# Performance work log

Hardware: AMD Instinct MI355X
Metric: run time of the kernel (lower is better)

Reference implementation:

```python
import jax, jax.numpy as jnp
import numpy as np

N_EMBD = 1024
N_HEAD = 16
HEAD_DIM = N_EMBD // N_HEAD  # 64
N_CTX = 2048
ROPE_THETA = 10000.0


def _rope_cache(L, dim, base):
    inv_freq = 1.0 / (base ** (np.arange(0, dim, 2, dtype=np.float32) / dim))
    t = np.arange(L, dtype=np.float32)
    freqs = np.einsum('i,j->ij', t, inv_freq)  # (L, dim/2)
    return jnp.asarray(np.cos(freqs)), jnp.asarray(np.sin(freqs))


def _apply_rotary(x, cos, sin):
    # x: (B, H, L, D), cos/sin: (L, D/2) -> broadcast (1,1,L,D/2)
    x1 = x[..., ::2]
    x2 = x[..., 1::2]
    c = cos[None, None, :, :]
    s = sin[None, None, :, :]
    y1 = x1 * c - x2 * s
    y2 = x1 * s + x2 * c
    # interleave back: stack on last dim then flatten
    return jnp.stack((y1, y2), axis=-1).reshape(x.shape)


def setup_inputs() -> dict:
    key = jax.random.key(0)
    k1, k2, k3, k4, k5 = jax.random.split(key, 5)
    B, L, D = 4, 2048, N_EMBD
    scale = 0.02
    x = jax.random.normal(k1, (B, L, D), dtype=jnp.float32)
    W_qkv = jax.random.normal(k2, (D, 3 * D), dtype=jnp.float32) * scale
    b_qkv = jnp.zeros((3 * D,), dtype=jnp.float32)
    W_proj = jax.random.normal(k3, (D, D), dtype=jnp.float32) * scale
    b_proj = jnp.zeros((D,), dtype=jnp.float32)
    attention_mask = jnp.ones((B, L), dtype=jnp.int32)
    return {"x": x, "W_qkv": W_qkv, "b_qkv": b_qkv, "W_proj": W_proj,
            "b_proj": b_proj, "attention_mask": attention_mask}


def reference(x, W_qkv, b_qkv, W_proj, b_proj, attention_mask):
    B, L, D = x.shape
    H, Dh = N_HEAD, HEAD_DIM
    qkv = x @ W_qkv + b_qkv  # (B, L, 3D)
    q, k, v = jnp.split(qkv, 3, axis=2)
    # (B, L, H, Dh) -> (B, H, L, Dh)
    q = q.reshape(B, L, H, Dh).transpose(0, 2, 1, 3)
    k = k.reshape(B, L, H, Dh).transpose(0, 2, 1, 3)
    v = v.reshape(B, L, H, Dh).transpose(0, 2, 1, 3)
    cos, sin = _rope_cache(L, Dh, ROPE_THETA)
    q = _apply_rotary(q, cos, sin)
    k = _apply_rotary(k, cos, sin)
    # mask: causal & key padding keep
    causal = jnp.tril(jnp.ones((L, L), dtype=bool))[None, None]        # (1,1,L,L)
    key_keep = attention_mask.astype(bool)[:, None, None, :]          # (B,1,1,L)
    keep = causal & key_keep                                          # (B,1,L,L)
    scores = jnp.einsum('bhqd,bhkd->bhqk', q, k) / jnp.sqrt(jnp.float32(Dh))
    scores = jnp.where(keep, scores, jnp.finfo(scores.dtype).min)
    attn = jax.nn.softmax(scores, axis=-1)
    out = jnp.einsum('bhqk,bhkd->bhqd', attn, v)  # (B,H,L,Dh)
    out = out.transpose(0, 2, 1, 3).reshape(B, L, D)
    return out @ W_proj + b_proj
```

## Files before the change

kernel.cpp:

```cpp
#include <hip/hip_runtime.h>
#include <math.h>

typedef __bf16 bf16x8 __attribute__((ext_vector_type(8)));
typedef float f32x4 __attribute__((ext_vector_type(4)));
typedef float f32x16 __attribute__((ext_vector_type(16)));
typedef unsigned short u16;
typedef unsigned short u16x8 __attribute__((ext_vector_type(8)));
typedef unsigned short u16x4 __attribute__((ext_vector_type(4)));
typedef unsigned u32x2v __attribute__((ext_vector_type(2)));

#define BATCH 4
#define SEQ   2048
#define EMBD  1024
#define NHEAD 16
#define HDIM  64
#define MROWS 8192
#define QKVN  3072

__device__ __forceinline__ u16 f2bf(float f) {
    union { float f; unsigned u; } cv; cv.f = f;
    unsigned u = cv.u;
    return (u16)((u + 0x7FFFu + ((u >> 16) & 1u)) >> 16);
}

__device__ __forceinline__ unsigned cvtpk_bf16(float lo, float hi) {
    unsigned r;
    asm("v_cvt_pk_bf16_f32 %0, %1, %2" : "=v"(r) : "v"(lo), "v"(hi));
    return r;
}

__device__ __forceinline__ void glds16(const void* g, void* l) {
    __builtin_amdgcn_global_load_lds(
        (const __attribute__((address_space(1))) unsigned int*)(g),
        (__attribute__((address_space(3))) unsigned int*)(l), 16, 0, 0);
}

__device__ __forceinline__ void transpose_body(const float* __restrict__ W,
                                               u16* __restrict__ Wt, int K, int N,
                                               int n0, int k0, u16 (*T)[68]) {
    const int tx = threadIdx.x & 15, ty = threadIdx.x >> 4;
#pragma unroll
    for (int r = 0; r < 4; r++) {
        int k = k0 + ty + r * 16;
        float4 w = *(const float4*)&W[(size_t)k * N + n0 + tx * 4];
        T[tx * 4 + 0][ty + r * 16] = f2bf(w.x);
        T[tx * 4 + 1][ty + r * 16] = f2bf(w.y);
        T[tx * 4 + 2][ty + r * 16] = f2bf(w.z);
        T[tx * 4 + 3][ty + r * 16] = f2bf(w.w);
    }
    __syncthreads();
#pragma unroll
    for (int r = 0; r < 4; r++) {
        int nl = ty + r * 16;
        u16x4 v = { T[nl][tx * 4 + 0], T[nl][tx * 4 + 1],
                    T[nl][tx * 4 + 2], T[nl][tx * 4 + 3] };
        *(u16x4*)&Wt[(size_t)(n0 + nl) * K + k0 + tx * 4] = v;
    }
}

__global__ __launch_bounds__(256)
void prep_kernel(const float* __restrict__ x, const float* __restrict__ Wqkv,
                 const float* __restrict__ Wproj, const int* __restrict__ amask,
                 u16* __restrict__ Xb, u16* __restrict__ Wqkvt, u16* __restrict__ Wprojt,
                 float* __restrict__ ropeC, float* __restrict__ ropeS,
                 float* __restrict__ mbias, int* __restrict__ flags) {
    __shared__ union { u16 T[64][68]; int ok[4]; } sm;
    const int bx = blockIdx.x, tid = threadIdx.x;
    if (bx < 8192) {
        int i = bx * 256 + tid;
        float4 v = ((const float4*)x)[i];
        u16x4 o = { f2bf(v.x), f2bf(v.y), f2bf(v.z), f2bf(v.w) };
        ((u16x4*)Xb)[i] = o;
    } else if (bx < 8960) {
        int bxx = bx - 8192;
        transpose_body(Wqkv, Wqkvt, EMBD, QKVN, (bxx % 48) * 64, (bxx / 48) * 64, sm.T);
    } else if (bx < 9216) {
        int bxx = bx - 8960;
        transpose_body(Wproj, Wprojt, EMBD, EMBD, (bxx & 15) * 64, (bxx >> 4) * 64, sm.T);
    } else if (bx < 9472) {
        int i = (bx - 9216) * 256 + tid;
        int l = i >> 5, p = i & 31;
        float invf = powf(10000.0f, -(float)(2 * p) * (1.0f / 64.0f));
        float sv, cv;
        sincosf((float)l * invf, &sv, &cv);
        ropeC[i] = cv; ropeS[i] = sv;
    } else {
        int idx = (bx - 9472) * 256 + tid;
        int mv = amask[idx];
        mbias[idx] = mv ? 0.0f : -1e30f;
        unsigned long long bal = __ballot(mv != 0);
        int wv = tid >> 6;
        if ((tid & 63) == 0) sm.ok[wv] = (bal == 0xFFFFFFFFFFFFFFFFull);
        __syncthreads();
        if (tid == 0)   flags[idx >> 7] = sm.ok[0] & sm.ok[1];
        if (tid == 128) flags[idx >> 7] = sm.ok[2] & sm.ok[3];
    }
}

__global__ __launch_bounds__(256)
void qkv_gemm(const u16* __restrict__ A, const u16* __restrict__ Bt,
              const float* __restrict__ bias,
              const float* __restrict__ Ct, const float* __restrict__ St,
              u16* __restrict__ Qo, u16* __restrict__ Ko, u16* __restrict__ Vo) {
    __shared__ u16 As[128 * 32];
    __shared__ u16 Bs[128 * 32];
    const int tid = threadIdx.x;
    const int wv = tid >> 6, ln = tid & 63;
    const int quad = ln >> 4, l16 = ln & 15;
    const int m0 = blockIdx.y * 128, n0 = blockIdx.x * 128;
    const int wm = wv >> 1, wn = wv & 1;

    f32x4 acc[4][4] = {};
    for (int k0 = 0; k0 < EMBD; k0 += 32) {
#pragma unroll
        for (int p = 0; p < 2; p++) {
            int slot = p * 256 + tid;
            int row = slot >> 2, ch = slot & 3;
            glds16(A  + (size_t)(m0 + row) * EMBD + k0 + ch * 8, As + (p * 256 + wv * 64) * 8);
            glds16(Bt + (size_t)(n0 + row) * EMBD + k0 + ch * 8, Bs + (p * 256 + wv * 64) * 8);
        }
        __syncthreads();
        bf16x8 af[4], bfr[4];
#pragma unroll
        for (int i = 0; i < 4; i++) af[i]  = *(const bf16x8*)&As[(wm * 64 + i * 16 + l16) * 32 + quad * 8];
#pragma unroll
        for (int j = 0; j < 4; j++) bfr[j] = *(const bf16x8*)&Bs[(wn * 64 + j * 16 + l16) * 32 + quad * 8];
#pragma unroll
        for (int i = 0; i < 4; i++)
#pragma unroll
            for (int j = 0; j < 4; j++)
                acc[i][j] = __builtin_amdgcn_mfma_f32_16x16x32_bf16(af[i], bfr[j], acc[i][j], 0, 0, 0);
        __syncthreads();
    }

    const int sec = n0 >> 10;
    if (sec == 2) {
#pragma unroll
        for (int i = 0; i < 4; i++)
#pragma unroll
            for (int r = 0; r < 4; r++) {
                int m = m0 + wm * 64 + i * 16 + quad * 4 + r;
                int b = m >> 11, l = m & 2047;
#pragma unroll
                for (int j = 0; j < 4; j++) {
                    int n = n0 + wn * 64 + j * 16 + l16;
                    int dcol = n & 1023;
                    int h = dcol >> 6, dh = dcol & 63;
                    float v = acc[i][j][r] + bias[n];
                    Vo[(((size_t)b * NHEAD + h) * SEQ + l) * HDIM + dh] = f2bf(v);
                }
            }
    } else {
        u16* O = (sec == 0) ? Qo : Ko;
        const float qs = (sec == 0) ? 0.125f * 1.44269504f : 1.0f;
#pragma unroll
        for (int i = 0; i < 4; i++)
#pragma unroll
            for (int r = 0; r < 4; r++) {
                int m = m0 + wm * 64 + i * 16 + quad * 4 + r;
                int b = m >> 11, l = m & 2047;
#pragma unroll
                for (int j = 0; j < 4; j++) {
                    int n = n0 + wn * 64 + j * 16 + l16;
                    int h = (n & 1023) >> 6, dh = n & 63;
                    int p = (n & 63) >> 1;
                    float v = acc[i][j][r] + bias[n];
                    float pv = __shfl_xor(v, 1, 64);
                    float cv = Ct[l * 32 + p], sv = St[l * 32 + p];
                    float o = (l16 & 1) ? (pv * sv + v * cv) : (v * cv - pv * sv);
                    O[(((size_t)b * NHEAD + h) * SEQ + l) * HDIM + dh] = f2bf(o * qs);
                }
            }
    }
}

__global__ __launch_bounds__(256)
void transpose_v(const u16* __restrict__ Vo, u16* __restrict__ Vt) {
    __shared__ u16 T[64][72];
    const int bh = blockIdx.y;
    const int l0 = blockIdx.x * 64;
    const int tx = threadIdx.x & 15, ty = threadIdx.x >> 4;
#pragma unroll
    for (int rr = 0; rr < 4; rr++) {
        int l = ty + rr * 16;
        u16x4 v = *(const u16x4*)&Vo[((size_t)bh * SEQ + l0 + l) * HDIM + tx * 4];
        T[l][tx * 4 + 0] = v.x; T[l][tx * 4 + 1] = v.y;
        T[l][tx * 4 + 2] = v.z; T[l][tx * 4 + 3] = v.w;
    }
    __syncthreads();
#pragma unroll
    for (int rr = 0; rr < 4; rr++) {
        int dh = ty + rr * 16;
        u16x4 w = { T[tx * 4 + 0][dh], T[tx * 4 + 1][dh],
                    T[tx * 4 + 2][dh], T[tx * 4 + 3][dh] };
        *(u16x4*)&Vt[((size_t)bh * HDIM + dh) * SEQ + l0 + tx * 4] = w;
    }
}

__global__ __launch_bounds__(256)
void attn_mfma3(const u16* __restrict__ Qb, const u16* __restrict__ Kb,
                const u16* __restrict__ Vt, const float* __restrict__ mb,
                const int* __restrict__ flags, u16* __restrict__ Ot) {
    __shared__ u16 SM[32768];
    const int tid = threadIdx.x;
    const int wv = tid >> 6, ln = tid & 63;
    const int l32 = ln & 31, hi = ln >> 5;
    const int bh = blockIdx.x & 63;
    const int pr = blockIdx.x >> 6;
    const int b = bh >> 4;
    const u16* Qg = Qb + (size_t)bh * SEQ * HDIM;
    const u16* Kg = Kb + (size_t)bh * SEQ * HDIM;
    const u16* Vg = Vt + (size_t)bh * HDIM * SEQ;

    const int kRow = ln >> 3;
    const size_t kLane = (size_t)(wv * 32 + kRow) * 64 + ((ln & 7) ^ kRow) * 8;
    const int vRow = ln >> 4, sc0 = (ln & 15) ^ vRow;
    const size_t vLaneE = (size_t)(wv * 16 + vRow) * SEQ + sc0 * 8;
    const size_t vLaneO = (size_t)(wv * 16 + vRow) * SEQ + (sc0 ^ 4) * 8;

    for (int pass = 0; pass < 2; pass++) {
        const int qt = pass ? pr : 15 - pr;
        const int q0w = qt * 128 + wv * 32;

        bf16x8 Qf[4];
#pragma unroll
        for (int kd = 0; kd < 4; kd++)
            Qf[kd] = *(const bf16x8*)&Qg[(size_t)(q0w + l32) * HDIM + kd * 16 + hi * 8];

        f32x16 o[2] = {};
        float mrun = -1e30f, lrun = 0.f;

        {
            u16* KsD = SM + wv * 2048;
            u16* VsD = SM + 8192 + wv * 2048;
#pragma unroll
            for (int p = 0; p < 4; p++) {
                glds16(Kg + kLane + p * 512, KsD + p * 512);
                glds16(Vg + ((p & 1) ? vLaneO : vLaneE) + (size_t)p * 4 * SEQ, VsD + p * 512);
            }
        }
        __syncthreads();

        int buf = 0;
        for (int kt = 0; kt <= qt; kt++) {
            const int kbase = kt * 128;
            if (kt < qt) {
                const size_t nb = (size_t)(kbase + 128);
                u16* KsD = SM + (buf ^ 1) * 16384 + wv * 2048;
                u16* VsD = SM + (buf ^ 1) * 16384 + 8192 + wv * 2048;
#pragma unroll
                for (int p = 0; p < 4; p++) {
                    glds16(Kg + nb * 64 + kLane + p * 512, KsD + p * 512);
                    glds16(Vg + nb + ((p & 1) ? vLaneO : vLaneE) + (size_t)p * 4 * SEQ, VsD + p * 512);
                }
            }
            const u16* Ks = SM + buf * 16384;
            const u16* Vs = SM + buf * 16384 + 8192;

            f32x16 s[4];
            __builtin_amdgcn_s_setprio(1);
#pragma unroll
            for (int mi = 0; mi < 4; mi++) {
                const int key = mi * 32 + l32;
                f32x16 z = {};
#pragma unroll
                for (int kd = 0; kd < 4; kd++) {
                    int ch = kd * 2 + hi;
                    bf16x8 kf = *(const bf16x8*)&Ks[key * 64 + ((ch ^ (key & 7)) * 8)];
                    z = __builtin_amdgcn_mfma_f32_32x32x16_bf16(kf, Qf[kd], z, 0, 0, 0);
                }
                s[mi] = z;
            }
            __builtin_amdgcn_s_setprio(0);

            if (kt == qt) {
                const int qloc = wv * 32 + l32;
#pragma unroll
                for (int mi = 0; mi < 4; mi++)
#pragma unroll
                    for (int r = 0; r < 16; r++) {
                        int row = mi * 32 + (r & 3) + 8 * (r >> 2) + 4 * hi;
                        if (row > qloc) s[mi][r] = -1e30f;
                    }
            }
            if (!flags[b * 16 + kt]) {
#pragma unroll
                for (int mi = 0; mi < 4; mi++)
#pragma unroll
                    for (int r = 0; r < 16; r++) {
                        int row = mi * 32 + (r & 3) + 8 * (r >> 2) + 4 * hi;
                        s[mi][r] += mb[b * SEQ + kbase + row];
                    }
            }

            float rm = -1e30f;
#pragma unroll
            for (int mi = 0; mi < 4; mi++) {
                float a0 = fmaxf(fmaxf(s[mi][0],  s[mi][1]),  fmaxf(s[mi][2],  s[mi][3]));
                float a1 = fmaxf(fmaxf(s[mi][4],  s[mi][5]),  fmaxf(s[mi][6],  s[mi][7]));
                float a2 = fmaxf(fmaxf(s[mi][8],  s[mi][9]),  fmaxf(s[mi][10], s[mi][11]));
                float a3 = fmaxf(fmaxf(s[mi][12], s[mi][13]), fmaxf(s[mi][14], s[mi][15]));
                rm = fmaxf(rm, fmaxf(fmaxf(a0, a1), fmaxf(a2, a3)));
            }
            {
                u32x2v f = __builtin_amdgcn_permlane32_swap(
                    __float_as_uint(rm), __float_as_uint(rm), false, false);
                rm = fmaxf(__uint_as_float(f[0]), __uint_as_float(f[1]));
            }
            if (!__all(rm <= mrun + 8.0f)) {
                float mnew = fmaxf(mrun, rm);
                float al = __builtin_amdgcn_exp2f(mrun - mnew);
                mrun = mnew;
                lrun *= al;
#pragma unroll
                for (int r = 0; r < 16; r++) { o[0][r] *= al; o[1][r] *= al; }
            }
            float rs = 0.f;
#pragma unroll
            for (int mi = 0; mi < 4; mi++) {
                float ps = 0.f;
#pragma unroll
                for (int r = 0; r < 16; r++) {
                    float pe = __builtin_amdgcn_exp2f(s[mi][r] - mrun);
                    s[mi][r] = pe;
                    ps += pe;
                }
                rs += ps;
            }
            {
                u32x2v f = __builtin_amdgcn_permlane32_swap(
                    __float_as_uint(rs), __float_as_uint(rs), false, false);
                rs = __uint_as_float(f[0]) + __uint_as_float(f[1]);
            }
            lrun += rs;

#pragma unroll
            for (int t = 0; t < 4; t++) {
                unsigned A0 = cvtpk_bf16(s[t][0],  s[t][1]);
                unsigned B0 = cvtpk_bf16(s[t][4],  s[t][5]);
                unsigned A1 = cvtpk_bf16(s[t][2],  s[t][3]);
                unsigned B1 = cvtpk_bf16(s[t][6],  s[t][7]);
                u32x2v r0 = __builtin_amdgcn_permlane32_swap(A0, B0, false, false);
                u32x2v r1 = __builtin_amdgcn_permlane32_swap(A1, B1, false, false);
                union { unsigned u[4]; bf16x8 v; } p0;
                p0.u[0] = r0[0]; p0.u[1] = r1[0]; p0.u[2] = r0[1]; p0.u[3] = r1[1];

                unsigned A2 = cvtpk_bf16(s[t][8],  s[t][9]);
                unsigned B2 = cvtpk_bf16(s[t][12], s[t][13]);
                unsigned A3 = cvtpk_bf16(s[t][10], s[t][11]);
                unsigned B3 = cvtpk_bf16(s[t][14], s[t][15]);
                u32x2v r2 = __builtin_amdgcn_permlane32_swap(A2, B2, false, false);
                u32x2v r3 = __builtin_amdgcn_permlane32_swap(A3, B3, false, false);
                union { unsigned u[4]; bf16x8 v; } p1;
                p1.u[0] = r2[0]; p1.u[1] = r3[0]; p1.u[2] = r2[1]; p1.u[3] = r3[1];

                __builtin_amdgcn_s_setprio(1);
#pragma unroll
                for (int md = 0; md < 2; md++) {
                    const int dh = md * 32 + l32;
                    bf16x8 v0 = *(const bf16x8*)&Vs[dh * 128 + (((t * 4 + hi)     ^ (dh & 7)) * 8)];
                    o[md] = __builtin_amdgcn_mfma_f32_32x32x16_bf16(v0, p0.v, o[md], 0, 0, 0);
                    bf16x8 v1 = *(const bf16x8*)&Vs[dh * 128 + (((t * 4 + 2 + hi) ^ (dh & 7)) * 8)];
                    o[md] = __builtin_amdgcn_mfma_f32_32x32x16_bf16(v1, p1.v, o[md], 0, 0, 0);
                }
                __builtin_amdgcn_s_setprio(0);
            }
            __syncthreads();
            buf ^= 1;
        }

        u16* Osh = SM + wv * 2176;
        float inv = 1.0f / lrun;
#pragma unroll
        for (int md = 0; md < 2; md++)
#pragma unroll
            for (int r = 0; r < 16; r++) {
                int dh = md * 32 + (r & 3) + 8 * (r >> 2) + 4 * hi;
                Osh[l32 * 68 + dh] = f2bf(o[md][r] * inv);
            }
        __syncthreads();
        {
            int qrow = ln >> 1, hf = ln & 1;
            size_t gbase = ((size_t)bh * SEQ + qt * 128 + wv * 32 + qrow) * HDIM + hf * 32;
#pragma unroll
            for (int c = 0; c < 4; c++) {
                u16x8 vv = *(const u16x8*)&Osh[qrow * 68 + hf * 32 + c * 8];
                *(u16x8*)&Ot[gbase + c * 8] = vv;
            }
        }
        __syncthreads();
    }
}

__global__ __launch_bounds__(256)
void proj_gemm(const u16* __restrict__ A, const u16* __restrict__ Bt,
               const float* __restrict__ bias, float* __restrict__ out) {
    __shared__ u16 As[128 * 32];
    __shared__ u16 Bs[128 * 32];
    const int tid = threadIdx.x;
    const int wv = tid >> 6, ln = tid & 63;
    const int quad = ln >> 4, l16 = ln & 15;
    const int m0 = blockIdx.y * 128, n0 = blockIdx.x * 128;
    const int wm = wv >> 1, wn = wv & 1;

    f32x4 acc[4][4] = {};
    for (int k0 = 0; k0 < EMBD; k0 += 32) {
#pragma unroll
        for (int p = 0; p < 2; p++) {
            int slot = p * 256 + tid;
            int row = slot >> 2, ch = slot & 3;
            int m = m0 + row;
            int bb = m >> 11, l = m & 2047;
            int hh = k0 >> 6;
            glds16(A + (((size_t)(bb * 16 + hh) * SEQ + l) * HDIM) + (k0 & 63) + ch * 8,
                   As + (p * 256 + wv * 64) * 8);
            glds16(Bt + (size_t)(n0 + row) * EMBD + k0 + ch * 8, Bs + (p * 256 + wv * 64) * 8);
        }
        __syncthreads();
        bf16x8 af[4], bfr[4];
#pragma unroll
        for (int i = 0; i < 4; i++) af[i]  = *(const bf16x8*)&As[(wm * 64 + i * 16 + l16) * 32 + quad * 8];
#pragma unroll
        for (int j = 0; j < 4; j++) bfr[j] = *(const bf16x8*)&Bs[(wn * 64 + j * 16 + l16) * 32 + quad * 8];
#pragma unroll
        for (int i = 0; i < 4; i++)
#pragma unroll
            for (int j = 0; j < 4; j++)
                acc[i][j] = __builtin_amdgcn_mfma_f32_16x16x32_bf16(af[i], bfr[j], acc[i][j], 0, 0, 0);
        __syncthreads();
    }
#pragma unroll
    for (int i = 0; i < 4; i++)
#pragma unroll
        for (int r = 0; r < 4; r++) {
            int m = m0 + wm * 64 + i * 16 + quad * 4 + r;
#pragma unroll
            for (int j = 0; j < 4; j++) {
                int n = n0 + wn * 64 + j * 16 + l16;
                out[(size_t)m * EMBD + n] = acc[i][j][r] + bias[n];
            }
        }
}

extern "C" void kernel_launch(void* const* d_in, const int* in_sizes, int n_in,
                              void* d_out, int out_size, void* d_ws, size_t ws_size,
                              hipStream_t stream)
{
    const float* x     = (const float*)d_in[0];
    const float* Wqkv  = (const float*)d_in[1];
    const float* bqkv  = (const float*)d_in[2];
    const float* Wproj = (const float*)d_in[3];
    const float* bproj = (const float*)d_in[4];
    const int*   amask = (const int*)d_in[5];
    float* out = (float*)d_out;

    char* ws = (char*)d_ws;
    u16*   Xb     = (u16*)(ws);
    u16*   Ot     = (u16*)(ws);
    u16*   Wqkvt  = (u16*)(ws + 16777216);
    u16*   Wprojt = (u16*)(ws + 23068672);
    u16*   Qb     = (u16*)(ws + 25165824);
    u16*   Kb     = (u16*)(ws + 41943040);
    u16*   Vb     = (u16*)(ws + 58720256);
    u16*   Vtp    = (u16*)(ws + 75497472);
    float* ropeC  = (float*)(ws + 92274688);
    float* ropeS  = (float*)(ws + 92536832);
    float* mbias  = (float*)(ws + 92798976);
    int*   flags  = (int*)(ws + 92831744);

    prep_kernel<<<9504, 256, 0, stream>>>(x, Wqkv, Wproj, amask,
                                          Xb, Wqkvt, Wprojt, ropeC, ropeS, mbias, flags);
    qkv_gemm<<<dim3(QKVN / 128, MROWS / 128), 256, 0, stream>>>(
        Xb, Wqkvt, bqkv, ropeC, ropeS, Qb, Kb, Vb);
    transpose_v<<<dim3(32, 64), 256, 0, stream>>>(Vb, Vtp);
    attn_mfma3<<<512, 256, 0, stream>>>(Qb, Kb, Vtp, mbias, flags, Ot);
    proj_gemm<<<dim3(EMBD / 128, MROWS / 128), 256, 0, stream>>>(Ot, Wprojt, bproj, out);
}
```

Measured before the change: 278.9 us.

## Double-buffer GEMM K-tiles with XOR-swizzled LDS and block-index swizzle

```diff
diff --git a/kernel.cpp b/kernel.cpp
--- a/kernel.cpp
+++ b/kernel.cpp
@@ -102,35 +102,61 @@
               const float* __restrict__ bias,
               const float* __restrict__ Ct, const float* __restrict__ St,
               u16* __restrict__ Qo, u16* __restrict__ Ko, u16* __restrict__ Vo) {
-    __shared__ u16 As[128 * 32];
-    __shared__ u16 Bs[128 * 32];
+    __shared__ u16 SM[32768];
     const int tid = threadIdx.x;
     const int wv = tid >> 6, ln = tid & 63;
     const int quad = ln >> 4, l16 = ln & 15;
-    const int m0 = blockIdx.y * 128, n0 = blockIdx.x * 128;
+    const int bid = blockIdx.y * 24 + blockIdx.x;
+    const int swz = (bid & 7) * 192 + (bid >> 3);
+    const int m0 = (swz / 24) * 128, n0 = (swz % 24) * 128;
     const int wm = wv >> 1, wn = wv & 1;
 
+    const int srow = wv * 8 + (ln >> 3);
+    const int xs = (ln & 7) ^ (srow & 7);
+
     f32x4 acc[4][4] = {};
-    for (int k0 = 0; k0 < EMBD; k0 += 32) {
-#pragma unroll
-        for (int p = 0; p < 2; p++) {
-            int slot = p * 256 + tid;
-            int row = slot >> 2, ch = slot & 3;
-            glds16(A  + (size_t)(m0 + row) * EMBD + k0 + ch * 8, As + (p * 256 + wv * 64) * 8);
-            glds16(Bt + (size_t)(n0 + row) * EMBD + k0 + ch * 8, Bs + (p * 256 + wv * 64) * 8);
-        }
+
+    auto stage = [&](int buf, int k0) {
+        u16* As = SM + buf * 16384;
+        u16* Bs = As + 8192;
+#pragma unroll
+        for (int p = 0; p < 4; p++) {
+            int row = p * 32 + srow;
+            glds16(A  + (size_t)(m0 + row) * EMBD + k0 + xs * 8, As + (p * 256 + wv * 64) * 8);
+            glds16(Bt + (size_t)(n0 + row) * EMBD + k0 + xs * 8, Bs + (p * 256 + wv * 64) * 8);
+        }
+    };
+
+    stage(0, 0);
+    __syncthreads();
+    int buf = 0;
+    for (int kt = 0; kt < 16; kt++) {
+        if (kt < 15) stage(buf ^ 1, (kt + 1) * 64);
+        const u16* As = SM + buf * 16384;
+        const u16* Bs = As + 8192;
+        __builtin_amdgcn_s_setprio(1);
+#pragma unroll
+        for (int kk = 0; kk < 2; kk++) {
+            bf16x8 af[4], bfr[4];
+#pragma unroll
+            for (int i = 0; i < 4; i++) {
+                int R = wm * 64 + i * 16 + l16;
+                af[i] = *(const bf16x8*)&As[R * 64 + (((kk * 4 + quad) ^ (R & 7)) * 8)];
+            }
+#pragma unroll
+            for (int j = 0; j < 4; j++) {
+                int R = wn * 64 + j * 16 + l16;
+                bfr[j] = *(const bf16x8*)&Bs[R * 64 + (((kk * 4 + quad) ^ (R & 7)) * 8)];
+            }
+#pragma unroll
+            for (int i = 0; i < 4; i++)
+#pragma unroll
+                for (int j = 0; j < 4; j++)
+                    acc[i][j] = __builtin_amdgcn_mfma_f32_16x16x32_bf16(af[i], bfr[j], acc[i][j], 0, 0, 0);
+        }
+        __builtin_amdgcn_s_setprio(0);
         __syncthreads();
-        bf16x8 af[4], bfr[4];
-#pragma unroll
-        for (int i = 0; i < 4; i++) af[i]  = *(const bf16x8*)&As[(wm * 64 + i * 16 + l16) * 32 + quad * 8];
-#pragma unroll
-        for (int j = 0; j < 4; j++) bfr[j] = *(const bf16x8*)&Bs[(wn * 64 + j * 16 + l16) * 32 + quad * 8];
-#pragma unroll
-        for (int i = 0; i < 4; i++)
-#pragma unroll
-            for (int j = 0; j < 4; j++)
-                acc[i][j] = __builtin_amdgcn_mfma_f32_16x16x32_bf16(af[i], bfr[j], acc[i][j], 0, 0, 0);
-        __syncthreads();
+        buf ^= 1;
     }
 
     const int sec = n0 >> 10;
@@ -395,39 +421,65 @@
 __global__ __launch_bounds__(256)
 void proj_gemm(const u16* __restrict__ A, const u16* __restrict__ Bt,
                const float* __restrict__ bias, float* __restrict__ out) {
-    __shared__ u16 As[128 * 32];
-    __shared__ u16 Bs[128 * 32];
+    __shared__ u16 SM[32768];
     const int tid = threadIdx.x;
     const int wv = tid >> 6, ln = tid & 63;
     const int quad = ln >> 4, l16 = ln & 15;
-    const int m0 = blockIdx.y * 128, n0 = blockIdx.x * 128;
+    const int bid = blockIdx.y * 8 + blockIdx.x;
+    const int swz = (bid & 7) * 64 + (bid >> 3);
+    const int m0 = (swz >> 3) * 128, n0 = (swz & 7) * 128;
     const int wm = wv >> 1, wn = wv & 1;
 
+    const int srow = wv * 8 + (ln >> 3);
+    const int xs = (ln & 7) ^ (srow & 7);
+
     f32x4 acc[4][4] = {};
-    for (int k0 = 0; k0 < EMBD; k0 += 32) {
-#pragma unroll
-        for (int p = 0; p < 2; p++) {
-            int slot = p * 256 + tid;
-            int row = slot >> 2, ch = slot & 3;
+
+    auto stage = [&](int buf, int kt) {
+        u16* As = SM + buf * 16384;
+        u16* Bs = As + 8192;
+#pragma unroll
+        for (int p = 0; p < 4; p++) {
+            int row = p * 32 + srow;
             int m = m0 + row;
             int bb = m >> 11, l = m & 2047;
-            int hh = k0 >> 6;
-            glds16(A + (((size_t)(bb * 16 + hh) * SEQ + l) * HDIM) + (k0 & 63) + ch * 8,
+            glds16(A + (((size_t)(bb * 16 + kt) * SEQ + l) * HDIM) + xs * 8,
                    As + (p * 256 + wv * 64) * 8);
-            glds16(Bt + (size_t)(n0 + row) * EMBD + k0 + ch * 8, Bs + (p * 256 + wv * 64) * 8);
-        }
+            glds16(Bt + (size_t)(n0 + row) * EMBD + kt * 64 + xs * 8,
+                   Bs + (p * 256 + wv * 64) * 8);
+        }
+    };
+
+    stage(0, 0);
+    __syncthreads();
+    int buf = 0;
+    for (int kt = 0; kt < 16; kt++) {
+        if (kt < 15) stage(buf ^ 1, kt + 1);
+        const u16* As = SM + buf * 16384;
+        const u16* Bs = As + 8192;
+        __builtin_amdgcn_s_setprio(1);
+#pragma unroll
+        for (int kk = 0; kk < 2; kk++) {
+            bf16x8 af[4], bfr[4];
+#pragma unroll
+            for (int i = 0; i < 4; i++) {
+                int R = wm * 64 + i * 16 + l16;
+                af[i] = *(const bf16x8*)&As[R * 64 + (((kk * 4 + quad) ^ (R & 7)) * 8)];
+            }
+#pragma unroll
+            for (int j = 0; j < 4; j++) {
+                int R = wn * 64 + j * 16 + l16;
+                bfr[j] = *(const bf16x8*)&Bs[R * 64 + (((kk * 4 + quad) ^ (R & 7)) * 8)];
+            }
+#pragma unroll
+            for (int i = 0; i < 4; i++)
+#pragma unroll
+                for (int j = 0; j < 4; j++)
+                    acc[i][j] = __builtin_amdgcn_mfma_f32_16x16x32_bf16(af[i], bfr[j], acc[i][j], 0, 0, 0);
+        }
+        __builtin_amdgcn_s_setprio(0);
         __syncthreads();
-        bf16x8 af[4], bfr[4];
-#pragma unroll
-        for (int i = 0; i < 4; i++) af[i]  = *(const bf16x8*)&As[(wm * 64 + i * 16 + l16) * 32 + quad * 8];
-#pragma unroll
-        for (int j = 0; j < 4; j++) bfr[j] = *(const bf16x8*)&Bs[(wn * 64 + j * 16 + l16) * 32 + quad * 8];
-#pragma unroll
-        for (int i = 0; i < 4; i++)
-#pragma unroll
-            for (int j = 0; j < 4; j++)
-                acc[i][j] = __builtin_amdgcn_mfma_f32_16x16x32_bf16(af[i], bfr[j], acc[i][j], 0, 0, 0);
-        __syncthreads();
+        buf ^= 1;
     }
 #pragma unroll
     for (int i = 0; i < 4; i++)
```

Result: faster. 251.0 us (-10.0%).

## Rewrite QKV and projection GEMMs with 256x128 tiles, double-buffered swizzled LDS pipeline

Applied to the files above, without the earlier changes.

```diff
diff --git a/kernel.cpp b/kernel.cpp
--- a/kernel.cpp
+++ b/kernel.cpp
@@ -34,6 +34,16 @@
         (const __attribute__((address_space(1))) unsigned int*)(g),
         (__attribute__((address_space(3))) unsigned int*)(l), 16, 0, 0);
 }
+
+#define MF8(qm, A0, A1, A2, A3, B0, B1)                                          \
+    acc[(qm)*4+0][0] = __builtin_amdgcn_mfma_f32_16x16x32_bf16(A0, B0, acc[(qm)*4+0][0], 0, 0, 0); \
+    acc[(qm)*4+0][1] = __builtin_amdgcn_mfma_f32_16x16x32_bf16(A0, B1, acc[(qm)*4+0][1], 0, 0, 0); \
+    acc[(qm)*4+1][0] = __builtin_amdgcn_mfma_f32_16x16x32_bf16(A1, B0, acc[(qm)*4+1][0], 0, 0, 0); \
+    acc[(qm)*4+1][1] = __builtin_amdgcn_mfma_f32_16x16x32_bf16(A1, B1, acc[(qm)*4+1][1], 0, 0, 0); \
+    acc[(qm)*4+2][0] = __builtin_amdgcn_mfma_f32_16x16x32_bf16(A2, B0, acc[(qm)*4+2][0], 0, 0, 0); \
+    acc[(qm)*4+2][1] = __builtin_amdgcn_mfma_f32_16x16x32_bf16(A2, B1, acc[(qm)*4+2][1], 0, 0, 0); \
+    acc[(qm)*4+3][0] = __builtin_amdgcn_mfma_f32_16x16x32_bf16(A3, B0, acc[(qm)*4+3][0], 0, 0, 0); \
+    acc[(qm)*4+3][1] = __builtin_amdgcn_mfma_f32_16x16x32_bf16(A3, B1, acc[(qm)*4+3][1], 0, 0, 0);
 
 __device__ __forceinline__ void transpose_body(const float* __restrict__ W,
                                                u16* __restrict__ Wt, int K, int N,
@@ -97,56 +107,106 @@
     }
 }
 
-__global__ __launch_bounds__(256)
+__global__ __launch_bounds__(512, 2)
 void qkv_gemm(const u16* __restrict__ A, const u16* __restrict__ Bt,
               const float* __restrict__ bias,
               const float* __restrict__ Ct, const float* __restrict__ St,
               u16* __restrict__ Qo, u16* __restrict__ Ko, u16* __restrict__ Vo) {
-    __shared__ u16 As[128 * 32];
-    __shared__ u16 Bs[128 * 32];
+    __shared__ u16 SM[49152];
     const int tid = threadIdx.x;
-    const int wv = tid >> 6, ln = tid & 63;
+    const int w = tid >> 6, ln = tid & 63;
     const int quad = ln >> 4, l16 = ln & 15;
-    const int m0 = blockIdx.y * 128, n0 = blockIdx.x * 128;
-    const int wm = wv >> 1, wn = wv & 1;
-
-    f32x4 acc[4][4] = {};
-    for (int k0 = 0; k0 < EMBD; k0 += 32) {
-#pragma unroll
-        for (int p = 0; p < 2; p++) {
-            int slot = p * 256 + tid;
-            int row = slot >> 2, ch = slot & 3;
-            glds16(A  + (size_t)(m0 + row) * EMBD + k0 + ch * 8, As + (p * 256 + wv * 64) * 8);
-            glds16(Bt + (size_t)(n0 + row) * EMBD + k0 + ch * 8, Bs + (p * 256 + wv * 64) * 8);
-        }
-        __syncthreads();
-        bf16x8 af[4], bfr[4];
-#pragma unroll
-        for (int i = 0; i < 4; i++) af[i]  = *(const bf16x8*)&As[(wm * 64 + i * 16 + l16) * 32 + quad * 8];
-#pragma unroll
-        for (int j = 0; j < 4; j++) bfr[j] = *(const bf16x8*)&Bs[(wn * 64 + j * 16 + l16) * 32 + quad * 8];
-#pragma unroll
-        for (int i = 0; i < 4; i++)
-#pragma unroll
-            for (int j = 0; j < 4; j++)
-                acc[i][j] = __builtin_amdgcn_mfma_f32_16x16x32_bf16(af[i], bfr[j], acc[i][j], 0, 0, 0);
-        __syncthreads();
+    const int wm = w >> 2, wn = w & 3;
+    const int bid = blockIdx.y * 24 + blockIdx.x;
+    const int swz = (bid & 7) * 96 + (bid >> 3);
+    const int m0 = (swz / 24) * 256, n0 = (swz % 24) * 128;
+
+    const int sr8 = ln >> 3;
+    const int xs = (ln & 7) ^ sr8;
+    const u16* Ab = A  + (size_t)(m0 + w * 8 + sr8) * EMBD + xs * 8;
+    const u16* Bb = Bt + (size_t)(n0 + w * 8 + sr8) * EMBD + xs * 8;
+    u16* ldsA = SM + w * 512;
+    u16* ldsB = SM + 32768 + w * 512;
+    const int ch0 = ((0 + quad) ^ (l16 & 7)) * 8;
+    const int ch1 = ((4 + quad) ^ (l16 & 7)) * 8;
+
+    auto stageA = [&](int buf, int rb, int kt) {
+        glds16(Ab + (size_t)rb * EMBD + kt * 64, ldsA + buf * 16384 + rb * 64);
+    };
+    auto stageB = [&](int buf, int rb, int kt) {
+        glds16(Bb + (size_t)rb * EMBD + kt * 64, ldsB + buf * 8192 + rb * 64);
+    };
+
+    f32x4 acc[8][2] = {};
+
+    stageA(0, 0, 0);  stageA(0, 128, 0);
+    stageA(0, 64, 0); stageA(0, 192, 0);
+    stageB(0, 0, 0);  stageB(0, 64, 0);
+    stageA(1, 0, 1);  stageA(1, 128, 1);
+    asm volatile("s_waitcnt vmcnt(2)" ::: "memory");
+    __builtin_amdgcn_sched_barrier(0);
+    __builtin_amdgcn_s_barrier();
+
+    for (int u = 0; u < 16; ++u) {
+        const int c = u & 1, nc = c ^ 1;
+        const u16* Ac0 = SM + c * 16384 + (wm * 128 + l16) * 64;
+        const u16* Ac1 = Ac0 + 64 * 64;
+        const u16* Bc  = SM + 32768 + c * 8192 + (wn * 32 + l16) * 64;
+        bf16x8 a0, a1, a2, a3, bk0a, bk0b, bk1a, bk1b;
+        a0 = *(const bf16x8*)&Ac0[ch0];        a1 = *(const bf16x8*)&Ac0[1024 + ch0];
+        a2 = *(const bf16x8*)&Ac0[2048 + ch0]; a3 = *(const bf16x8*)&Ac0[3072 + ch0];
+        bk0a = *(const bf16x8*)&Bc[ch0];       bk0b = *(const bf16x8*)&Bc[1024 + ch0];
+        if (u < 15) { stageA(nc, 64, u + 1); stageA(nc, 192, u + 1); stageB(nc, 64, u + 1); }
+        __builtin_amdgcn_sched_barrier(0);
+        __builtin_amdgcn_s_setprio(1);
+        MF8(0, a0, a1, a2, a3, bk0a, bk0b);
+        __builtin_amdgcn_s_setprio(0);
+        __builtin_amdgcn_sched_barrier(0);
+        a0 = *(const bf16x8*)&Ac0[ch1];        a1 = *(const bf16x8*)&Ac0[1024 + ch1];
+        a2 = *(const bf16x8*)&Ac0[2048 + ch1]; a3 = *(const bf16x8*)&Ac0[3072 + ch1];
+        bk1a = *(const bf16x8*)&Bc[ch1];       bk1b = *(const bf16x8*)&Bc[1024 + ch1];
+        if (u < 15) stageB(nc, 0, u + 1);
+        __builtin_amdgcn_sched_barrier(0);
+        __builtin_amdgcn_s_setprio(1);
+        MF8(0, a0, a1, a2, a3, bk1a, bk1b);
+        __builtin_amdgcn_s_setprio(0);
+        __builtin_amdgcn_sched_barrier(0);
+        __builtin_amdgcn_s_barrier();
+        a0 = *(const bf16x8*)&Ac1[ch0];        a1 = *(const bf16x8*)&Ac1[1024 + ch0];
+        a2 = *(const bf16x8*)&Ac1[2048 + ch0]; a3 = *(const bf16x8*)&Ac1[3072 + ch0];
+        if (u < 14) { stageA(c, 0, u + 2); stageA(c, 128, u + 2); }
+        __builtin_amdgcn_sched_barrier(0);
+        __builtin_amdgcn_s_setprio(1);
+        MF8(1, a0, a1, a2, a3, bk0a, bk0b);
+        __builtin_amdgcn_s_setprio(0);
+        __builtin_amdgcn_sched_barrier(0);
+        a0 = *(const bf16x8*)&Ac1[ch1];        a1 = *(const bf16x8*)&Ac1[1024 + ch1];
+        a2 = *(const bf16x8*)&Ac1[2048 + ch1]; a3 = *(const bf16x8*)&Ac1[3072 + ch1];
+        __builtin_amdgcn_sched_barrier(0);
+        __builtin_amdgcn_s_setprio(1);
+        MF8(1, a0, a1, a2, a3, bk1a, bk1b);
+        __builtin_amdgcn_s_setprio(0);
+        __builtin_amdgcn_sched_barrier(0);
+        if (u < 14) asm volatile("s_waitcnt vmcnt(2)" ::: "memory");
+        else        asm volatile("s_waitcnt vmcnt(0)" ::: "memory");
+        __builtin_amdgcn_sched_barrier(0);
+        __builtin_amdgcn_s_barrier();
     }
 
     const int sec = n0 >> 10;
     if (sec == 2) {
 #pragma unroll
-        for (int i = 0; i < 4; i++)
+        for (int ii = 0; ii < 8; ii++)
 #pragma unroll
             for (int r = 0; r < 4; r++) {
-                int m = m0 + wm * 64 + i * 16 + quad * 4 + r;
+                int m = m0 + wm * 128 + ii * 16 + quad * 4 + r;
                 int b = m >> 11, l = m & 2047;
 #pragma unroll
-                for (int j = 0; j < 4; j++) {
-                    int n = n0 + wn * 64 + j * 16 + l16;
+                for (int j = 0; j < 2; j++) {
+                    int n = n0 + wn * 32 + j * 16 + l16;
                     int dcol = n & 1023;
                     int h = dcol >> 6, dh = dcol & 63;
-                    float v = acc[i][j][r] + bias[n];
+                    float v = acc[ii][j][r] + bias[n];
                     Vo[(((size_t)b * NHEAD + h) * SEQ + l) * HDIM + dh] = f2bf(v);
                 }
             }
@@ -154,17 +214,17 @@
         u16* O = (sec == 0) ? Qo : Ko;
         const float qs = (sec == 0) ? 0.125f * 1.44269504f : 1.0f;
 #pragma unroll
-        for (int i = 0; i < 4; i++)
+        for (int ii = 0; ii < 8; ii++)
 #pragma unroll
             for (int r = 0; r < 4; r++) {
-                int m = m0 + wm * 64 + i * 16 + quad * 4 + r;
+                int m = m0 + wm * 128 + ii * 16 + quad * 4 + r;
                 int b = m >> 11, l = m & 2047;
 #pragma unroll
-                for (int j = 0; j < 4; j++) {
-                    int n = n0 + wn * 64 + j * 16 + l16;
+                for (int j = 0; j < 2; j++) {
+                    int n = n0 + wn * 32 + j * 16 + l16;
                     int h = (n & 1023) >> 6, dh = n & 63;
                     int p = (n & 63) >> 1;
-                    float v = acc[i][j][r] + bias[n];
+                    float v = acc[ii][j][r] + bias[n];
                     float pv = __shfl_xor(v, 1, 64);
                     float cv = Ct[l * 32 + p], sv = St[l * 32 + p];
                     float o = (l16 & 1) ? (pv * sv + v * cv) : (v * cv - pv * sv);
@@ -392,52 +452,102 @@
     }
 }
 
-__global__ __launch_bounds__(256)
+__global__ __launch_bounds__(512, 2)
 void proj_gemm(const u16* __restrict__ A, const u16* __restrict__ Bt,
                const float* __restrict__ bias, float* __restrict__ out) {
-    __shared__ u16 As[128 * 32];
-    __shared__ u16 Bs[128 * 32];
+    __shared__ u16 SM[49152];
     const int tid = threadIdx.x;
-    const int wv = tid >> 6, ln = tid & 63;
+    const int w = tid >> 6, ln = tid & 63;
     const int quad = ln >> 4, l16 = ln & 15;
-    const int m0 = blockIdx.y * 128, n0 = blockIdx.x * 128;
-    const int wm = wv >> 1, wn = wv & 1;
-
-    f32x4 acc[4][4] = {};
-    for (int k0 = 0; k0 < EMBD; k0 += 32) {
-#pragma unroll
-        for (int p = 0; p < 2; p++) {
-            int slot = p * 256 + tid;
-            int row = slot >> 2, ch = slot & 3;
-            int m = m0 + row;
-            int bb = m >> 11, l = m & 2047;
-            int hh = k0 >> 6;
-            glds16(A + (((size_t)(bb * 16 + hh) * SEQ + l) * HDIM) + (k0 & 63) + ch * 8,
-                   As + (p * 256 + wv * 64) * 8);
-            glds16(Bt + (size_t)(n0 + row) * EMBD + k0 + ch * 8, Bs + (p * 256 + wv * 64) * 8);
-        }
-        __syncthreads();
-        bf16x8 af[4], bfr[4];
-#pragma unroll
-        for (int i = 0; i < 4; i++) af[i]  = *(const bf16x8*)&As[(wm * 64 + i * 16 + l16) * 32 + quad * 8];
-#pragma unroll
-        for (int j = 0; j < 4; j++) bfr[j] = *(const bf16x8*)&Bs[(wn * 64 + j * 16 + l16) * 32 + quad * 8];
-#pragma unroll
-        for (int i = 0; i < 4; i++)
-#pragma unroll
-            for (int j = 0; j < 4; j++)
-                acc[i][j] = __builtin_amdgcn_mfma_f32_16x16x32_bf16(af[i], bfr[j], acc[i][j], 0, 0, 0);
-        __syncthreads();
-    }
-#pragma unroll
-    for (int i = 0; i < 4; i++)
+    const int wm = w >> 2, wn = w & 3;
+    const int bid = blockIdx.y * 8 + blockIdx.x;
+    const int swz = (bid & 7) * 32 + (bid >> 3);
+    const int m0 = (swz >> 3) * 256, n0 = (swz & 7) * 128;
+
+    const int sr8 = ln >> 3;
+    const int xs = (ln & 7) ^ sr8;
+    const int aRow = m0 + w * 8 + sr8;
+    const int bb16 = (aRow >> 11) * 16;
+    const int lrow = aRow & 2047;
+    const u16* Ap = A + ((size_t)bb16 * SEQ + lrow) * HDIM + xs * 8;
+    const u16* Bb = Bt + (size_t)(n0 + w * 8 + sr8) * EMBD + xs * 8;
+    u16* ldsA = SM + w * 512;
+    u16* ldsB = SM + 32768 + w * 512;
+    const int ch0 = ((0 + quad) ^ (l16 & 7)) * 8;
+    const int ch1 = ((4 + quad) ^ (l16 & 7)) * 8;
+
+    auto stageA = [&](int buf, int rb, int kt) {
+        glds16(Ap + ((size_t)kt * SEQ + rb) * HDIM, ldsA + buf * 16384 + rb * 64);
+    };
+    auto stageB = [&](int buf, int rb, int kt) {
+        glds16(Bb + (size_t)rb * EMBD + kt * 64, ldsB + buf * 8192 + rb * 64);
+    };
+
+    f32x4 acc[8][2] = {};
+
+    stageA(0, 0, 0);  stageA(0, 128, 0);
+    stageA(0, 64, 0); stageA(0, 192, 0);
+    stageB(0, 0, 0);  stageB(0, 64, 0);
+    stageA(1, 0, 1);  stageA(1, 128, 1);
+    asm volatile("s_waitcnt vmcnt(2)" ::: "memory");
+    __builtin_amdgcn_sched_barrier(0);
+    __builtin_amdgcn_s_barrier();
+
+    for (int u = 0; u < 16; ++u) {
+        const int c = u & 1, nc = c ^ 1;
+        const u16* Ac0 = SM + c * 16384 + (wm * 128 + l16) * 64;
+        const u16* Ac1 = Ac0 + 64 * 64;
+        const u16* Bc  = SM + 32768 + c * 8192 + (wn * 32 + l16) * 64;
+        bf16x8 a0, a1, a2, a3, bk0a, bk0b, bk1a, bk1b;
+        a0 = *(const bf16x8*)&Ac0[ch0];        a1 = *(const bf16x8*)&Ac0[1024 + ch0];
+        a2 = *(const bf16x8*)&Ac0[2048 + ch0]; a3 = *(const bf16x8*)&Ac0[3072 + ch0];
+        bk0a = *(const bf16x8*)&Bc[ch0];       bk0b = *(const bf16x8*)&Bc[1024 + ch0];
+        if (u < 15) { stageA(nc, 64, u + 1); stageA(nc, 192, u + 1); stageB(nc, 64, u + 1); }
+        __builtin_amdgcn_sched_barrier(0);
+        __builtin_amdgcn_s_setprio(1);
+        MF8(0, a0, a1, a2, a3, bk0a, bk0b);
+        __builtin_amdgcn_s_setprio(0);
+        __builtin_amdgcn_sched_barrier(0);
+        a0 = *(const bf16x8*)&Ac0[ch1];        a1 = *(const bf16x8*)&Ac0[1024 + ch1];
+        a2 = *(const bf16x8*)&Ac0[2048 + ch1]; a3 = *(const bf16x8*)&Ac0[3072 + ch1];
+        bk1a = *(const bf16x8*)&Bc[ch1];       bk1b = *(const bf16x8*)&Bc[1024 + ch1];
+        if (u < 15) stageB(nc, 0, u + 1);
+        __builtin_amdgcn_sched_barrier(0);
+        __builtin_amdgcn_s_setprio(1);
+        MF8(0, a0, a1, a2, a3, bk1a, bk1b);
+        __builtin_amdgcn_s_setprio(0);
+        __builtin_amdgcn_sched_barrier(0);
+        __builtin_amdgcn_s_barrier();
+        a0 = *(const bf16x8*)&Ac1[ch0];        a1 = *(const bf16x8*)&Ac1[1024 + ch0];
+        a2 = *(const bf16x8*)&Ac1[2048 + ch0]; a3 = *(const bf16x8*)&Ac1[3072 + ch0];
+        if (u < 14) { stageA(c, 0, u + 2); stageA(c, 128, u + 2); }
+        __builtin_amdgcn_sched_barrier(0);
+        __builtin_amdgcn_s_setprio(1);
+        MF8(1, a0, a1, a2, a3, bk0a, bk0b);
+        __builtin_amdgcn_s_setprio(0);
+        __builtin_amdgcn_sched_barrier(0);
+        a0 = *(const bf16x8*)&Ac1[ch1];        a1 = *(const bf16x8*)&Ac1[1024 + ch1];
+        a2 = *(const bf16x8*)&Ac1[2048 + ch1]; a3 = *(const bf16x8*)&Ac1[3072 + ch1];
+        __builtin_amdgcn_sched_barrier(0);
+        __builtin_amdgcn_s_setprio(1);
+        MF8(1, a0, a1, a2, a3, bk1a, bk1b);
+        __builtin_amdgcn_s_setprio(0);
+        __builtin_amdgcn_sched_barrier(0);
+        if (u < 14) asm volatile("s_waitcnt vmcnt(2)" ::: "memory");
+        else        asm volatile("s_waitcnt vmcnt(0)" ::: "memory");
+        __builtin_amdgcn_sched_barrier(0);
+        __builtin_amdgcn_s_barrier();
+    }
+
+#pragma unroll
+    for (int ii = 0; ii < 8; ii++)
 #pragma unroll
         for (int r = 0; r < 4; r++) {
-            int m = m0 + wm * 64 + i * 16 + quad * 4 + r;
-#pragma unroll
-            for (int j = 0; j < 4; j++) {
-                int n = n0 + wn * 64 + j * 16 + l16;
-                out[(size_t)m * EMBD + n] = acc[i][j][r] + bias[n];
+            int m = m0 + wm * 128 + ii * 16 + quad * 4 + r;
+#pragma unroll
+            for (int j = 0; j < 2; j++) {
+                int n = n0 + wn * 32 + j * 16 + l16;
+                out[(size_t)m * EMBD + n] = acc[ii][j][r] + bias[n];
             }
         }
 }
@@ -470,9 +580,9 @@
 
     prep_kernel<<<9504, 256, 0, stream>>>(x, Wqkv, Wproj, amask,
                                           Xb, Wqkvt, Wprojt, ropeC, ropeS, mbias, flags);
-    qkv_gemm<<<dim3(QKVN / 128, MROWS / 128), 256, 0, stream>>>(
+    qkv_gemm<<<dim3(24, 32), 512, 0, stream>>>(
         Xb, Wqkvt, bqkv, ropeC, ropeS, Qb, Kb, Vb);
     transpose_v<<<dim3(32, 64), 256, 0, stream>>>(Vb, Vtp);
     attn_mfma3<<<512, 256, 0, stream>>>(Qb, Kb, Vtp, mbias, flags, Ot);
-    proj_gemm<<<dim3(EMBD / 128, MROWS / 128), 256, 0, stream>>>(Ot, Wprojt, bproj, out);
-}
+    proj_gemm<<<dim3(8, 32), 512, 0, stream>>>(Ot, Wprojt, bproj, out);
+}
```

New measurement: 255.8 us. -8.3%, faster.
